# Kernel tuning notes

Hardware: AMD Instinct MI355X
Metric: run time of the kernel (lower is better)

The kernel has to match this reference:

```python
import jax, jax.numpy as jnp
import numpy as np

TEMPERATURE = 0.5
EPS = 1e-8  # matches torch CosineSimilarity eps


def setup_inputs() -> dict:
    key = jax.random.key(0)
    k1, k2 = jax.random.split(key)
    N, D = 4096, 256
    z1 = jax.random.normal(k1, (N, D), dtype=jnp.float32)
    z2 = jax.random.normal(k2, (N, D), dtype=jnp.float32)
    return {"z1": z1, "z2": z2}


def reference(z1, z2):
    N = z1.shape[0]
    z = jnp.concatenate([z1, z2], axis=0)            # [2N, D]
    norm = jnp.linalg.norm(z, axis=-1, keepdims=True)
    zn = z / jnp.maximum(norm, EPS)                  # L2-normalized
    sim = (zn @ zn.T) / TEMPERATURE                  # [2N, 2N] cosine sim / temp
    # mask self-similarity on the diagonal
    diag = jnp.eye(2 * N, dtype=bool)
    sim = jnp.where(diag, -jnp.inf, sim)
    # positive pair labels: row i pairs with i+N (first half) or i-N (second half)
    labels = jnp.concatenate([jnp.arange(N) + N, jnp.arange(N)])
    logp = jax.nn.log_softmax(sim, axis=-1)
    loss = -jnp.mean(logp[jnp.arange(2 * N), labels])
    return loss
```

## Files before the change

### kernel.cpp

```cpp
#include <hip/hip_runtime.h>
#include <hip/hip_bf16.h>


#define NROWS 8192
#define NHALF 4096
#define DDIM  256

typedef __bf16 bf16;
typedef __bf16 bf16x4 __attribute__((ext_vector_type(4)));
typedef __bf16 bf16x8 __attribute__((ext_vector_type(8)));
typedef float  f32x4  __attribute__((ext_vector_type(4)));

__constant__ const float kTwoLog2e = 2.8853900817779268f;
__constant__ const float kLn2      = 0.6931471805599453f;

__device__ __forceinline__ const float* zrow(const float* z1, const float* z2, int r) {
  return (r < NHALF) ? (z1 + (size_t)r * DDIM) : (z2 + (size_t)(r - NHALF) * DDIM);
}

__global__ void k_normalize(const float* __restrict__ z1, const float* __restrict__ z2,
                            bf16* __restrict__ zn, float* __restrict__ invn,
                            float* __restrict__ rowsum) {
  const int wave = threadIdx.x >> 6, lane = threadIdx.x & 63;
  const int row = blockIdx.x * 4 + wave;
  const float* src = zrow(z1, z2, row);
  f32x4 v = *(const f32x4*)(src + lane * 4);
  float ss = v.x * v.x + v.y * v.y + v.z * v.z + v.w * v.w;
#pragma unroll
  for (int off = 1; off < 64; off <<= 1) ss += __shfl_xor(ss, off);
  const float inv = 1.0f / fmaxf(sqrtf(ss), 1e-8f);
  bf16x4 o;
  o.x = (bf16)(v.x * inv); o.y = (bf16)(v.y * inv);
  o.z = (bf16)(v.z * inv); o.w = (bf16)(v.w * inv);
  *(bf16x4*)(zn + (size_t)row * DDIM + lane * 4) = o;
  if (lane == 0) { invn[row] = inv; rowsum[row] = 0.0f; }
}

#define BM 256
#define BN 64
#define CSPLIT 8
#define LDSB 528

__global__ __launch_bounds__(512, 2) void k_gram(const bf16* __restrict__ zn,
                                                 float* __restrict__ rowsum) {
  __shared__ __align__(16) unsigned char lds[2][BN * LDSB];
  const int tid  = threadIdx.x;
  const int wave = tid >> 6, lane = tid & 63;
  const int quad = lane >> 4, l15 = lane & 15;
  const int rowblk = blockIdx.x >> 3, csplit = blockIdx.x & 7;
  const int c0 = csplit * (NROWS / CSPLIT);
  const int iters = (NROWS / CSPLIT) / BN;

  bf16x8 a[2][8];
#pragma unroll
  for (int s = 0; s < 2; ++s) {
    const int row = rowblk * BM + wave * 32 + s * 16 + l15;
    const bf16x8* ap = (const bf16x8*)(zn + (size_t)row * DDIM);
#pragma unroll
    for (int k = 0; k < 8; ++k) a[s][k] = ap[k * 4 + quad];
  }

  const int tr = tid >> 3;
  const int tc = tid & 7;

  uint4 g[4];
  {
    const unsigned char* gp = (const unsigned char*)(zn + (size_t)(c0 + tr) * DDIM);
#pragma unroll
    for (int j = 0; j < 4; ++j) g[j] = *(const uint4*)(gp + (tc + 8 * j) * 16);
  }
#pragma unroll
  for (int j = 0; j < 4; ++j)
    *(uint4*)(&lds[0][tr * LDSB + (tc + 8 * j) * 16]) = g[j];

  float sum[2][4] = {{0.f, 0.f, 0.f, 0.f}, {0.f, 0.f, 0.f, 0.f}};
  const f32x4 zero4 = {0.f, 0.f, 0.f, 0.f};

  for (int it = 0; it < iters; ++it) {
    __syncthreads();
    const int cur = it & 1;
    if (it + 1 < iters) {
      const unsigned char* gp =
          (const unsigned char*)(zn + (size_t)(c0 + (it + 1) * BN + tr) * DDIM);
#pragma unroll
      for (int j = 0; j < 4; ++j) g[j] = *(const uint4*)(gp + (tc + 8 * j) * 16);
    }

    f32x4 acc[2][4];
#pragma unroll
    for (int s = 0; s < 2; ++s)
#pragma unroll
      for (int cs = 0; cs < 4; ++cs) acc[s][cs] = zero4;

#pragma unroll
    for (int k = 0; k < 8; ++k) {
      bf16x8 b[4];
#pragma unroll
      for (int cs = 0; cs < 4; ++cs)
        b[cs] = *(const bf16x8*)(&lds[cur][(cs * 16 + l15) * LDSB + k * 64 + quad * 16]);
#pragma unroll
      for (int s = 0; s < 2; ++s)
#pragma unroll
        for (int cs = 0; cs < 4; ++cs)
          acc[s][cs] = __builtin_amdgcn_mfma_f32_16x16x32_bf16(a[s][k], b[cs], acc[s][cs], 0, 0, 0);
    }

#pragma unroll
    for (int s = 0; s < 2; ++s)
#pragma unroll
      for (int cs = 0; cs < 4; ++cs)
#pragma unroll
        for (int r = 0; r < 4; ++r)
          sum[s][r] += __builtin_amdgcn_exp2f(acc[s][cs][r] * kTwoLog2e);

    if (it + 1 < iters) {
#pragma unroll
      for (int j = 0; j < 4; ++j)
        *(uint4*)(&lds[(it + 1) & 1][tr * LDSB + (tc + 8 * j) * 16]) = g[j];
    }
  }

#pragma unroll
  for (int s = 0; s < 2; ++s)
#pragma unroll
    for (int r = 0; r < 4; ++r) {
      float v = sum[s][r];
      v += __shfl_xor(v, 1); v += __shfl_xor(v, 2);
      v += __shfl_xor(v, 4); v += __shfl_xor(v, 8);
      if (l15 == 0) {
        const int row = rowblk * BM + wave * 32 + s * 16 + quad * 4 + r;
        atomicAdd(&rowsum[row], v);
      }
    }
}

__global__ void k_finalize(const float* __restrict__ z1, const float* __restrict__ z2,
                           const bf16* __restrict__ zn, const float* __restrict__ invn,
                           const float* __restrict__ rowsum, float* __restrict__ contrib) {
  const int wave = threadIdx.x >> 6, lane = threadIdx.x & 63;
  const int row = blockIdx.x * 4 + wave;
  const int pr = (row < NHALF) ? row + NHALF : row - NHALF;

  f32x4 a4 = *(const f32x4*)(zrow(z1, z2, row) + lane * 4);
  f32x4 b4 = *(const f32x4*)(zrow(z1, z2, pr) + lane * 4);
  bf16x4 nb = *(const bf16x4*)(zn + (size_t)row * DDIM + lane * 4);

  float pd = a4.x * b4.x + a4.y * b4.y + a4.z * b4.z + a4.w * b4.w;
  float f0 = (float)nb.x, f1 = (float)nb.y, f2 = (float)nb.z, f3 = (float)nb.w;
  float nd = f0 * f0 + f1 * f1 + f2 * f2 + f3 * f3;
#pragma unroll
  for (int off = 1; off < 64; off <<= 1) {
    pd += __shfl_xor(pd, off);
    nd += __shfl_xor(nd, off);
  }
  if (lane == 0) {
    const float p = 2.0f * pd * invn[row] * invn[pr];
    const float dexp = __builtin_amdgcn_exp2f(kTwoLog2e * nd);
    const float lse = __builtin_amdgcn_logf(rowsum[row] - dexp) * kLn2;
    contrib[row] = lse - p;
  }
}

__global__ void k_reduce(const float* __restrict__ contrib, float* __restrict__ out) {
  const int wave = threadIdx.x >> 6, lane = threadIdx.x & 63;
  float acc = 0.0f;
  for (int i = threadIdx.x; i < NROWS; i += 256) acc += contrib[i];
#pragma unroll
  for (int off = 1; off < 64; off <<= 1) acc += __shfl_xor(acc, off);
  __shared__ float wsum[4];
  if (lane == 0) wsum[wave] = acc;
  __syncthreads();
  if (threadIdx.x == 0)
    out[0] = (wsum[0] + wsum[1] + wsum[2] + wsum[3]) * (1.0f / (float)NROWS);
}

extern "C" void kernel_launch(void* const* d_in, const int* in_sizes, int n_in,
                              void* d_out, int out_size, void* d_ws, size_t ws_size,
                              hipStream_t stream) {
  const float* z1 = (const float*)d_in[0];
  const float* z2 = (const float*)d_in[1];
  unsigned char* ws = (unsigned char*)d_ws;

  bf16* zn = (bf16*)ws;
  float* invn = (float*)(ws + (size_t)NROWS * DDIM * sizeof(bf16));
  float* rowsum = invn + NROWS;
  float* contrib = rowsum + NROWS;

  hipLaunchKernelGGL(k_normalize, dim3(NROWS / 4), dim3(256), 0, stream, z1, z2, zn, invn, rowsum);
  hipLaunchKernelGGL(k_gram, dim3((NROWS / BM) * CSPLIT), dim3(512), 0, stream, zn, rowsum);
  hipLaunchKernelGGL(k_finalize, dim3(NROWS / 4), dim3(256), 0, stream, z1, z2, zn, invn, rowsum,
                     contrib);
  hipLaunchKernelGGL(k_reduce, dim3(1), dim3(256), 0, stream, contrib, (float*)d_out);
}
```

Baseline: 108.0 us.

## Stage Gram column tiles via direct global-to-LDS loads with XOR swizzle

The Gram kernel now loads B column tiles straight into LDS with global_load_lds, using an XOR-swizzled layout instead of padded rows staged through registers. Each wave covers 64 rows (4 A fragments) against 32-column tiles, with 256-thread blocks and a 16-way column split. The aim is to free VGPRs and VALU work spent on staging, avoid LDS bank conflicts, and raise A-fragment reuse per B load. In exchange there are more blocks and more atomics on rowsum, smaller tiles per iteration, and each wave holds 64 registers of A fragments.

Result: no change. 110.0 us (+1.8%).

```diff
diff --git a/kernel.cpp b/kernel.cpp
--- a/kernel.cpp
+++ b/kernel.cpp
@@ -36,101 +36,109 @@
   if (lane == 0) { invn[row] = inv; rowsum[row] = 0.0f; }
 }
 
-#define BM 256
-#define BN 64
-#define CSPLIT 8
-#define LDSB 528
-
-__global__ __launch_bounds__(512, 2) void k_gram(const bf16* __restrict__ zn,
+#define BMG 256
+#define BNG 32
+#define CSPLIT 16
+
+typedef const __attribute__((address_space(1))) unsigned int* as1_u32p;
+typedef __attribute__((address_space(3))) unsigned int* as3_u32p;
+
+__device__ __forceinline__ void load_lds16(const void* g, void* l) {
+  __builtin_amdgcn_global_load_lds((as1_u32p)g, (as3_u32p)l, 16, 0, 0);
+}
+
+__global__ __launch_bounds__(256, 2) void k_gram(const bf16* __restrict__ zn,
                                                  float* __restrict__ rowsum) {
-  __shared__ __align__(16) unsigned char lds[2][BN * LDSB];
+  __shared__ __align__(16) unsigned char ldsb[2][BNG * 512];
   const int tid  = threadIdx.x;
   const int wave = tid >> 6, lane = tid & 63;
   const int quad = lane >> 4, l15 = lane & 15;
-  const int rowblk = blockIdx.x >> 3, csplit = blockIdx.x & 7;
+  const int rowblk = blockIdx.x >> 4, csplit = blockIdx.x & 15;
   const int c0 = csplit * (NROWS / CSPLIT);
-  const int iters = (NROWS / CSPLIT) / BN;
-
-  bf16x8 a[2][8];
-#pragma unroll
-  for (int s = 0; s < 2; ++s) {
-    const int row = rowblk * BM + wave * 32 + s * 16 + l15;
-    const bf16x8* ap = (const bf16x8*)(zn + (size_t)row * DDIM);
-#pragma unroll
-    for (int k = 0; k < 8; ++k) a[s][k] = ap[k * 4 + quad];
-  }
-
-  const int tr = tid >> 3;
-  const int tc = tid & 7;
-
-  uint4 g[4];
+  const int iters = (NROWS / CSPLIT) / BNG;
+
   {
-    const unsigned char* gp = (const unsigned char*)(zn + (size_t)(c0 + tr) * DDIM);
-#pragma unroll
-    for (int j = 0; j < 4; ++j) g[j] = *(const uint4*)(gp + (tc + 8 * j) * 16);
-  }
-#pragma unroll
-  for (int j = 0; j < 4; ++j)
-    *(uint4*)(&lds[0][tr * LDSB + (tc + 8 * j) * 16]) = g[j];
-
-  float sum[2][4] = {{0.f, 0.f, 0.f, 0.f}, {0.f, 0.f, 0.f, 0.f}};
+    const unsigned char* src0 = (const unsigned char*)(zn + (size_t)c0 * DDIM);
+#pragma unroll
+    for (int j = 0; j < 4; ++j) {
+      const int p = (wave * 4 + j) * 64 + lane;
+      const int r = p >> 5;
+      const int q = (p & 31) ^ (r & 7);
+      load_lds16(src0 + r * 512 + q * 16, &ldsb[0][(wave * 4 + j) * 1024]);
+    }
+  }
+
+  const int R0 = rowblk * BMG + wave * 64;
+  bf16x8 a[4][8];
+#pragma unroll
+  for (int s = 0; s < 4; ++s) {
+    const bf16x8* ap = (const bf16x8*)(zn + (size_t)(R0 + s * 16 + l15) * DDIM);
+#pragma unroll
+    for (int kk = 0; kk < 8; ++kk) a[s][kk] = ap[kk * 4 + quad];
+  }
+
+  float sum[4][4];
+#pragma unroll
+  for (int s = 0; s < 4; ++s)
+#pragma unroll
+    for (int r = 0; r < 4; ++r) sum[s][r] = 0.0f;
+
   const f32x4 zero4 = {0.f, 0.f, 0.f, 0.f};
 
   for (int it = 0; it < iters; ++it) {
     __syncthreads();
-    const int cur = it & 1;
+    const unsigned char* bp = ldsb[it & 1];
+
     if (it + 1 < iters) {
-      const unsigned char* gp =
-          (const unsigned char*)(zn + (size_t)(c0 + (it + 1) * BN + tr) * DDIM);
-#pragma unroll
-      for (int j = 0; j < 4; ++j) g[j] = *(const uint4*)(gp + (tc + 8 * j) * 16);
-    }
-
-    f32x4 acc[2][4];
-#pragma unroll
-    for (int s = 0; s < 2; ++s)
-#pragma unroll
-      for (int cs = 0; cs < 4; ++cs) acc[s][cs] = zero4;
-
-#pragma unroll
-    for (int k = 0; k < 8; ++k) {
-      bf16x8 b[4];
-#pragma unroll
-      for (int cs = 0; cs < 4; ++cs)
-        b[cs] = *(const bf16x8*)(&lds[cur][(cs * 16 + l15) * LDSB + k * 64 + quad * 16]);
-#pragma unroll
-      for (int s = 0; s < 2; ++s)
-#pragma unroll
-        for (int cs = 0; cs < 4; ++cs)
-          acc[s][cs] = __builtin_amdgcn_mfma_f32_16x16x32_bf16(a[s][k], b[cs], acc[s][cs], 0, 0, 0);
-    }
-
-#pragma unroll
-    for (int s = 0; s < 2; ++s)
-#pragma unroll
-      for (int cs = 0; cs < 4; ++cs)
-#pragma unroll
-        for (int r = 0; r < 4; ++r)
-          sum[s][r] += __builtin_amdgcn_exp2f(acc[s][cs][r] * kTwoLog2e);
-
-    if (it + 1 < iters) {
-#pragma unroll
-      for (int j = 0; j < 4; ++j)
-        *(uint4*)(&lds[(it + 1) & 1][tr * LDSB + (tc + 8 * j) * 16]) = g[j];
-    }
-  }
-
-#pragma unroll
-  for (int s = 0; s < 2; ++s)
+      const unsigned char* srcn =
+          (const unsigned char*)(zn + (size_t)(c0 + (it + 1) * BNG) * DDIM);
+#pragma unroll
+      for (int j = 0; j < 4; ++j) {
+        const int p = (wave * 4 + j) * 64 + lane;
+        const int r = p >> 5;
+        const int q = (p & 31) ^ (r & 7);
+        load_lds16(srcn + r * 512 + q * 16, &ldsb[(it + 1) & 1][(wave * 4 + j) * 1024]);
+      }
+    }
+
+    f32x4 acc[4][2];
+#pragma unroll
+    for (int s = 0; s < 4; ++s) { acc[s][0] = zero4; acc[s][1] = zero4; }
+
+#pragma unroll
+    for (int kk = 0; kk < 8; ++kk) {
+      bf16x8 b[2];
+#pragma unroll
+      for (int cs = 0; cs < 2; ++cs) {
+        const int rb = cs * 16 + l15;
+        const int q  = (kk * 4 + quad) ^ (rb & 7);
+        b[cs] = *(const bf16x8*)(bp + rb * 512 + q * 16);
+      }
+#pragma unroll
+      for (int s = 0; s < 4; ++s)
+#pragma unroll
+        for (int cs = 0; cs < 2; ++cs)
+          acc[s][cs] =
+              __builtin_amdgcn_mfma_f32_16x16x32_bf16(a[s][kk], b[cs], acc[s][cs], 0, 0, 0);
+    }
+
+#pragma unroll
+    for (int s = 0; s < 4; ++s)
+#pragma unroll
+      for (int r = 0; r < 4; ++r)
+        sum[s][r] += __builtin_amdgcn_exp2f(acc[s][0][r] * kTwoLog2e) +
+                     __builtin_amdgcn_exp2f(acc[s][1][r] * kTwoLog2e);
+  }
+
+#pragma unroll
+  for (int s = 0; s < 4; ++s)
 #pragma unroll
     for (int r = 0; r < 4; ++r) {
       float v = sum[s][r];
       v += __shfl_xor(v, 1); v += __shfl_xor(v, 2);
       v += __shfl_xor(v, 4); v += __shfl_xor(v, 8);
-      if (l15 == 0) {
-        const int row = rowblk * BM + wave * 32 + s * 16 + quad * 4 + r;
-        atomicAdd(&rowsum[row], v);
-      }
+      if (l15 == 0)
+        atomicAdd(&rowsum[R0 + s * 16 + quad * 4 + r], v);
     }
 }
 
@@ -187,7 +195,7 @@
   float* contrib = rowsum + NROWS;
 
   hipLaunchKernelGGL(k_normalize, dim3(NROWS / 4), dim3(256), 0, stream, z1, z2, zn, invn, rowsum);
-  hipLaunchKernelGGL(k_gram, dim3((NROWS / BM) * CSPLIT), dim3(512), 0, stream, zn, rowsum);
+  hipLaunchKernelGGL(k_gram, dim3((NROWS / BMG) * CSPLIT), dim3(256), 0, stream, zn, rowsum);
   hipLaunchKernelGGL(k_finalize, dim3(NROWS / 4), dim3(256), 0, stream, z1, z2, zn, invn, rowsum,
                      contrib);
   hipLaunchKernelGGL(k_reduce, dim3(1), dim3(256), 0, stream, contrib, (float*)d_out);
```
